# Kernel optimization log

Hardware: AMD Instinct MI355X
Metric: run time of the kernel (lower is better)

The kernel has to match this reference:

```python
import jax, jax.numpy as jnp
import numpy as np

N_FREQS = 6  # PositionEmbedding default used by LISA


def setup_inputs() -> dict:
    key = jax.random.key(0)
    ks = jax.random.split(key, 8)
    B, L, N, D, H = 8, 32768, 2048, 64, 256
    in_dim = 1 * (2 * N_FREQS + 1) + 3 * D  # 13 + 192 = 205

    def w(k, i, o):
        return jax.random.normal(k, (i, o), jnp.float32) * (1.0 / np.sqrt(i))

    return {
        "coord": jax.random.uniform(ks[0], (B, L, 1), jnp.float32),
        "latent": jax.random.normal(ks[1], (B, N, D), jnp.float32),
        "W0": w(ks[2], in_dim, H), "b0": jnp.zeros((H,), jnp.float32),
        "W1": w(ks[3], H, H), "b1": jnp.zeros((H,), jnp.float32),
        "W2": w(ks[4], H, H), "b2": jnp.zeros((H,), jnp.float32),
        "W3": w(ks[5], H, H), "b3": jnp.zeros((H,), jnp.float32),
        "W4": w(ks[6], H, 1), "b4": jnp.zeros((1,), jnp.float32),
    }


def reference(coord, latent, W0, b0, W1, b1, W2, b2, W3, b3, W4, b4):
    B, N, D = latent.shape
    # feat_unfold: concat shifted-prev / self / shifted-next along channels
    feat = jnp.swapaxes(latent, 1, 2)                                   # [B, D, N]
    feat_prev = jnp.concatenate([feat[:, :, :1], feat[:, :, :-1]], axis=2)
    feat_next = jnp.concatenate([feat[:, :, 1:], feat[:, :, -1:]], axis=2)
    feat = jnp.concatenate([feat_prev, feat, feat_next], axis=1)        # [B, 3D, N]

    # grid_sample(bilinear, padding_mode='border', align_corners=False) on a
    # 1-row image: y coordinate 0 hits row 0 exactly, so only x interpolates.
    # torch mapping: ix = ((gx + 1) * W - 1) / 2 with gx = coord*2 - 1
    ix = coord[..., 0] * N - 0.5                                        # [B, L]
    x0 = jnp.floor(ix)
    t = ix - x0                                                         # lerp weight
    i0 = jnp.clip(x0.astype(jnp.int32), 0, N - 1)                       # border clamp
    i1 = jnp.clip(x0.astype(jnp.int32) + 1, 0, N - 1)
    f0 = jnp.take_along_axis(feat, i0[:, None, :], axis=2)              # [B, 3D, L]
    f1 = jnp.take_along_axis(feat, i1[:, None, :], axis=2)
    sampled = (1.0 - t)[:, None, :] * f0 + t[:, None, :] * f1
    sampled = jnp.swapaxes(sampled, 1, 2)                               # [B, L, 3D]

    # positional encoding: [x, sin(f x), cos(f x) for f in 1,2,4,8,16,32]
    freqs = 2.0 ** jnp.arange(N_FREQS, dtype=jnp.float32)
    ang = coord * freqs                                                 # [B, L, 6]
    pe = jnp.stack([jnp.sin(ang), jnp.cos(ang)], axis=-1)
    pe = pe.reshape(ang.shape[0], ang.shape[1], 2 * N_FREQS)            # [B, L, 12]

    inp = jnp.concatenate([coord, pe, sampled], axis=-1)                # [B, L, 205]

    h = jax.nn.relu(inp @ W0 + b0)
    h = jax.nn.relu(h @ W1 + b1)
    h = jax.nn.relu(h @ W2 + b2)
    h = jax.nn.relu(h @ W3 + b3)
    return h @ W4 + b4                                                  # [B, L, 1]
```

## Files before the change

### kernel.cpp

```cpp
#include <hip/hip_runtime.h>
#include <hip/hip_bf16.h>

typedef unsigned short ushort_t;
typedef unsigned int uint_t;
typedef __attribute__((ext_vector_type(8))) short short8;
typedef __attribute__((ext_vector_type(4))) float float4v;
typedef __attribute__((ext_vector_type(4))) uint_t uint4v;

#define NLAT 2048
#define DLAT 64

#define PW_BASE 128
#define PW0_OFF 0
#define PW1_OFF 57344
#define PW2_OFF 122880
#define PW3_OFF 188416

__device__ __forceinline__ float b2f(ushort_t u) {
  union { uint_t i; float f; } v; v.i = ((uint_t)u) << 16; return v.f;
}
__device__ __forceinline__ ushort_t f2b(float f) {
  uint_t x = __float_as_uint(f);
  uint_t r = (x + 0x7fffu + ((x >> 16) & 1u)) >> 16;
  return (ushort_t)r;
}
__device__ __forceinline__ uint_t pack2(float lo, float hi) {
  float2 t; t.x = lo; t.y = hi;
  union { __hip_bfloat162 h; uint_t u; } cv;
  cv.h = __float22bfloat162_rn(t);
  return cv.u;
}
__device__ __forceinline__ int imin(int a, int b) { return a < b ? a : b; }
__device__ __forceinline__ int imax(int a, int b) { return a > b ? a : b; }

__device__ __forceinline__ float ldv(const float* p, long i)    { return p[i]; }
__device__ __forceinline__ float ldv(const ushort_t* p, long i) { return b2f(p[i]); }
__device__ __forceinline__ void stv(float* p, long i, float v)    { p[i] = v; }
__device__ __forceinline__ void stv(ushort_t* p, long i, float v) { p[i] = f2b(v); }

__device__ __forceinline__ float4 load4f(const float* p) { return *(const float4*)p; }
__device__ __forceinline__ float4 load4f(const ushort_t* p) {
  uint2 u = *(const uint2*)p;
  float4 r;
  r.x = b2f((ushort_t)(u.x & 0xffffu)); r.y = b2f((ushort_t)(u.x >> 16));
  r.z = b2f((ushort_t)(u.y & 0xffffu)); r.w = b2f((ushort_t)(u.y >> 16));
  return r;
}

__device__ __forceinline__ void aload(short8& dst, const ushort_t* a) {
  asm volatile("global_load_dwordx4 %0, %1, off" : "=v"(dst) : "v"(a));
}
__device__ __forceinline__ void dsread(short8& dst, const ushort_t* p) {
  asm volatile("ds_read_b128 %0, %1"
               : "=v"(dst)
               : "v"((const __attribute__((address_space(3))) ushort_t*)p));
}
template <int N>
__device__ __forceinline__ void vmwait() {
  if constexpr (N == 0)       asm volatile("s_waitcnt vmcnt(0)"  ::: "memory");
  else if constexpr (N == 4)  asm volatile("s_waitcnt vmcnt(4)"  ::: "memory");
  else if constexpr (N == 8)  asm volatile("s_waitcnt vmcnt(8)"  ::: "memory");
  else                        asm volatile("s_waitcnt vmcnt(12)" ::: "memory");
}
template <int N>
__device__ __forceinline__ void lgwait() {
  if constexpr (N == 0) asm volatile("s_waitcnt lgkmcnt(0)" ::: "memory");
  else                  asm volatile("s_waitcnt lgkmcnt(4)" ::: "memory");
}

__global__ void detect_mode(const ushort_t* __restrict__ lat, int* __restrict__ flag) {
  if (threadIdx.x == 0) *flag = 0;
  __syncthreads();
  int big = 0;
  for (int i = threadIdx.x; i < 1024; i += 64) {
    float v = b2f(lat[i]);
    if (!(fabsf(v) < 1e5f)) big = 1;
  }
  if (__any(big) && threadIdx.x == 0) *flag = 1;
}

template <typename TI>
__device__ __forceinline__ void pack_body(const TI* __restrict__ W0, const TI* __restrict__ W1,
                                          const TI* __restrict__ W2, const TI* __restrict__ W3,
                                          ushort_t* __restrict__ pw)
{
  int g = blockIdx.x * blockDim.x + threadIdx.x;
  if (g >= 31 * 1024) return;
  int lane = g & 63, q = lane >> 4;
  int mt   = (g >> 6) & 15;
  int ktg  = g >> 10;
  const TI* W; ushort_t* dst; int kt, KT; bool isw0 = false;
  if (ktg < 7)       { W = W0; dst = pw + PW0_OFF; kt = ktg;      KT = 7; isw0 = true; }
  else if (ktg < 15) { W = W1; dst = pw + PW1_OFF; kt = ktg - 7;  KT = 8; }
  else if (ktg < 23) { W = W2; dst = pw + PW2_OFF; kt = ktg - 15; KT = 8; }
  else               { W = W3; dst = pw + PW3_OFF; kt = ktg - 23; KT = 8; }
  int col = mt * 16 + (lane & 15);
  uint_t words[4];
#pragma unroll
  for (int h = 0; h < 4; ++h) {
    ushort_t vv[2];
#pragma unroll
    for (int e = 0; e < 2; ++e) {
      int j = 2 * h + e;
      int f = 32 * kt + 16 * (j >> 2) + 4 * q + (j & 3);
      int row = f;
      if (isw0) row = (f < 192) ? (13 + f) : (f == 192 ? 0 : (f <= 204 ? f - 192 : -1));
      vv[e] = (row >= 0) ? f2b(ldv(W, (long)row * 256 + col)) : (ushort_t)0;
    }
    words[h] = (uint_t)vv[0] | ((uint_t)vv[1] << 16);
  }
  uint4 o; o.x = words[0]; o.y = words[1]; o.z = words[2]; o.w = words[3];
  *(uint4*)(dst + ((size_t)(mt * KT + kt) * 64 + lane) * 8) = o;
}

__global__ void pack_w_u(const void* W0, const void* W1, const void* W2, const void* W3,
                         ushort_t* __restrict__ pw, const int* __restrict__ flag)
{
  if (*flag == 1)
    pack_body<float>((const float*)W0, (const float*)W1, (const float*)W2, (const float*)W3, pw);
  else
    pack_body<ushort_t>((const ushort_t*)W0, (const ushort_t*)W1, (const ushort_t*)W2, (const ushort_t*)W3, pw);
}

template <int KT, int BASE, int NEXTKT>
__device__ __forceinline__ void run_layer_fp(const ushort_t* __restrict__ pwl,
                                             const ushort_t* __restrict__ pwl_next,
                                             float4v (&acc)[4][4],
                                             const ushort_t* __restrict__ act,
                                             int lane, int wv, short8 (&Ar)[4][4])
{
#pragma unroll
  for (int m = 0; m < 4; ++m)
#pragma unroll
    for (int i = 0; i < 4; ++i)
      acc[m][i] = (float4v){0.f, 0.f, 0.f, 0.f};

  const ushort_t* abase = pwl + (((size_t)(4 * wv) * KT) * 64 + lane) * 8;
  const ushort_t* nbase = nullptr;
  if constexpr (NEXTKT > 0)
    nbase = pwl_next + (((size_t)(4 * wv) * NEXTKT) * 64 + lane) * 8;

  int boff[4];
#pragma unroll
  for (int i = 0; i < 4; ++i) boff[i] = (((wv + i) & 3) << 12) + (lane << 3);

  short8 B0[4], B1[4];
#pragma unroll
  for (int i = 0; i < 4; ++i) dsread(B0[i], act + boff[i]);

#pragma unroll
  for (int kt = 0; kt < KT; ++kt) {
    short8 (&Bc)[4] = (kt & 1) ? B1 : B0;
    short8 (&Bn)[4] = (kt & 1) ? B0 : B1;
    if (kt + 1 < KT) {
#pragma unroll
      for (int i = 0; i < 4; ++i) dsread(Bn[i], act + boff[i] + (kt + 1) * 512);
    }
    if (kt + 3 < KT) {
#pragma unroll
      for (int m = 0; m < 4; ++m)
        aload(Ar[(BASE + kt + 3) & 3][m], abase + (size_t)(m * KT + kt + 3) * 512);
    } else if constexpr (NEXTKT > 0) {
      const int nk = kt + 3 - KT;
#pragma unroll
      for (int m = 0; m < 4; ++m)
        aload(Ar[(BASE + kt + 3) & 3][m], nbase + (size_t)(m * NEXTKT + nk) * 512);
    }
    if (kt + 1 < KT) lgwait<4>(); else lgwait<0>();
    if (kt + 3 < KT || NEXTKT > 0) vmwait<12>();
    else if (kt == KT - 3)         vmwait<8>();
    else if (kt == KT - 2)         vmwait<4>();
    else                           vmwait<0>();
    __builtin_amdgcn_sched_barrier(0);
    short8 (&Ac)[4] = Ar[(BASE + kt) & 3];
    __builtin_amdgcn_s_setprio(1);
#pragma unroll
    for (int i = 0; i < 4; ++i) {
      acc[0][i] = __builtin_amdgcn_mfma_f32_16x16x32_bf16(Ac[0], Bc[i], acc[0][i], 0, 0, 0);
      acc[1][i] = __builtin_amdgcn_mfma_f32_16x16x32_bf16(Ac[1], Bc[i], acc[1][i], 0, 0, 0);
      acc[2][i] = __builtin_amdgcn_mfma_f32_16x16x32_bf16(Ac[2], Bc[i], acc[2][i], 0, 0, 0);
      acc[3][i] = __builtin_amdgcn_mfma_f32_16x16x32_bf16(Ac[3], Bc[i], acc[3][i], 0, 0, 0);
    }
    __builtin_amdgcn_s_setprio(0);
  }
}

__device__ __forceinline__ void convert_store(float4v (&acc)[4][4],
                                              ushort_t* __restrict__ actN,
                                              const float* __restrict__ bwl,
                                              int lane, int wv, int q)
{
#pragma unroll
  for (int p2 = 0; p2 < 2; ++p2) {
    const float4 bE = *(const float4*)&bwl[wv * 64 + p2 * 32 + 4 * q];
    const float4 bO = *(const float4*)&bwl[wv * 64 + p2 * 32 + 16 + 4 * q];
    const int kt = 2 * wv + p2;
#pragma unroll
    for (int i = 0; i < 4; ++i) {
      const int p = (wv + i) & 3;
      const float4v& aE = acc[2 * p2][i];
      const float4v& aO = acc[2 * p2 + 1][i];
      uint4 o;
      o.x = pack2(fmaxf(aE[0] + bE.x, 0.f), fmaxf(aE[1] + bE.y, 0.f));
      o.y = pack2(fmaxf(aE[2] + bE.z, 0.f), fmaxf(aE[3] + bE.w, 0.f));
      o.z = pack2(fmaxf(aO[0] + bO.x, 0.f), fmaxf(aO[1] + bO.y, 0.f));
      o.w = pack2(fmaxf(aO[2] + bO.z, 0.f), fmaxf(aO[3] + bO.w, 0.f));
      *(uint4*)&actN[(size_t)(p << 12) + kt * 512 + (lane << 3)] = o;
    }
  }
  asm volatile("s_waitcnt lgkmcnt(0)" ::: "memory");
  __builtin_amdgcn_s_barrier();
}

template <typename TI>
__device__ __forceinline__ void fused_body(
    const TI* __restrict__ coord, const TI* __restrict__ latent,
    const TI* __restrict__ bias0, const TI* __restrict__ bias1,
    const TI* __restrict__ bias2, const TI* __restrict__ bias3,
    const TI* __restrict__ W4,    const TI* __restrict__ b4,
    const ushort_t* __restrict__ pw, TI* __restrict__ out,
    ushort_t (*act)[4 * 8 * 64 * 8], float* bw)
{
  const int tid  = threadIdx.x;
  const int lane = tid & 63, q = lane >> 4, m15 = lane & 15;
  const int wv   = tid >> 6;
  const long pbase = (long)blockIdx.x * 64 + wv * 16 + m15;

  for (int i = tid; i < 1281; i += 256) {
    float v;
    if (i < 256)       v = ldv(bias0, i);
    else if (i < 512)  v = ldv(bias1, i - 256);
    else if (i < 768)  v = ldv(bias2, i - 512);
    else if (i < 1024) v = ldv(bias3, i - 768);
    else if (i < 1280) v = ldv(W4, i - 1024);
    else               v = ldv(b4, 0);
    bw[i] = v;
  }

  {
    const long p = pbase;
    float c   = ldv(coord, p);
    float ixv = c * 2048.0f - 0.5f;
    float x0f = floorf(ixv);
    float t   = ixv - x0f;
    int   x0  = (int)x0f;
    int   i0  = imin(imax(x0, 0), NLAT - 1);
    int   i1  = imin(imax(x0 + 1, 0), NLAT - 1);
    float w0 = 1.0f - t, w1 = t;
    int rows0[3] = { imax(i0 - 1, 0), i0, imin(i0 + 1, NLAT - 1) };
    int rows1[3] = { imax(i1 - 1, 0), i1, imin(i1 + 1, NLAT - 1) };
    const TI* lat = latent + (size_t)(p >> 15) * (NLAT * DLAT);
    uint4v hu[7];
#pragma unroll
    for (int tb = 0; tb < 12; ++tb) {
      int region = tb >> 2;
      int d0 = 16 * (tb & 3) + 4 * q;
      float4 a = load4f(lat + (long)rows0[region] * DLAT + d0);
      float4 b = load4f(lat + (long)rows1[region] * DLAT + d0);
      hu[tb >> 1][(tb & 1) * 2 + 0] = pack2(w0 * a.x + w1 * b.x, w0 * a.y + w1 * b.y);
      hu[tb >> 1][(tb & 1) * 2 + 1] = pack2(w0 * a.z + w1 * b.z, w0 * a.w + w1 * b.w);
    }
    float pv[4];
#pragma unroll
    for (int s = 0; s < 4; ++s) {
      int f = 192 + 4 * q + s;
      float v = 0.0f;
      if (f == 192) v = c;
      else if (f <= 204) {
        int i = f - 193;
        float fr = (float)(1 << (i >> 1));
        float ang = c * fr;
        v = (i & 1) ? __cosf(ang) : __sinf(ang);
      }
      pv[s] = v;
    }
    hu[6][0] = pack2(pv[0], pv[1]);
    hu[6][1] = pack2(pv[2], pv[3]);
    hu[6][2] = 0; hu[6][3] = 0;

#pragma unroll
    for (int kt = 0; kt < 7; ++kt)
      *(uint4v*)&act[0][((size_t)(wv * 8 + kt) * 64 + lane) * 8] = hu[kt];
  }
  __syncthreads();

  short8 Ar[4][4];
  {
    const ushort_t* abase = pw + PW0_OFF + (((size_t)(4 * wv) * 7) * 64 + lane) * 8;
#pragma unroll
    for (int s = 0; s < 3; ++s)
#pragma unroll
      for (int m = 0; m < 4; ++m)
        aload(Ar[s][m], abase + (size_t)(m * 7 + s) * 512);
  }

  float4v acc[4][4];

  run_layer_fp<7, 0, 8>(pw + PW0_OFF, pw + PW1_OFF, acc, act[0], lane, wv, Ar);
  convert_store(acc, act[1], bw + 0 * 256, lane, wv, q);
  run_layer_fp<8, 3, 8>(pw + PW1_OFF, pw + PW2_OFF, acc, act[1], lane, wv, Ar);
  convert_store(acc, act[0], bw + 1 * 256, lane, wv, q);
  run_layer_fp<8, 3, 8>(pw + PW2_OFF, pw + PW3_OFF, acc, act[0], lane, wv, Ar);
  convert_store(acc, act[1], bw + 2 * 256, lane, wv, q);
  run_layer_fp<8, 3, 0>(pw + PW3_OFF, nullptr,      acc, act[1], lane, wv, Ar);

  float psum[4] = {0.f, 0.f, 0.f, 0.f};
#pragma unroll
  for (int m = 0; m < 4; ++m) {
    const float4 b3v = *(const float4*)&bw[3 * 256 + wv * 64 + m * 16 + 4 * q];
    const float4 w4v = *(const float4*)&bw[1024 + wv * 64 + m * 16 + 4 * q];
#pragma unroll
    for (int i = 0; i < 4; ++i) {
      float v;
      v = fmaxf(acc[m][i][0] + b3v.x, 0.f); psum[i] += v * w4v.x;
      v = fmaxf(acc[m][i][1] + b3v.y, 0.f); psum[i] += v * w4v.y;
      v = fmaxf(acc[m][i][2] + b3v.z, 0.f); psum[i] += v * w4v.z;
      v = fmaxf(acc[m][i][3] + b3v.w, 0.f); psum[i] += v * w4v.w;
    }
  }
#pragma unroll
  for (int i = 0; i < 4; ++i) {
    psum[i] += __shfl_xor(psum[i], 16, 64);
    psum[i] += __shfl_xor(psum[i], 32, 64);
  }

  asm volatile("" ::: "memory");
  __builtin_amdgcn_s_barrier();
  float* part = (float*)act[0];
  if (lane < 16) {
#pragma unroll
    for (int i = 0; i < 4; ++i) {
      const int p = (wv + i) & 3;
      part[wv * 64 + p * 16 + lane] = psum[i];
    }
  }
  __syncthreads();
  if (tid < 64) {
    float s = part[tid] + part[64 + tid] + part[128 + tid] + part[192 + tid]
            + bw[1280];
    stv(out, (long)blockIdx.x * 64 + tid, s);
  }
}

__global__ __launch_bounds__(256, 2) void lisa_fused_u(
    const void* coord, const void* latent,
    const void* bias0, const void* bias1, const void* bias2, const void* bias3,
    const void* W4,    const void* b4,
    const ushort_t* __restrict__ pw, void* out, const int* __restrict__ flag)
{
  __shared__ __align__(16) ushort_t act[2][4 * 8 * 64 * 8];
  __shared__ __align__(16) float bw[4 * 256 + 256 + 1];

  if (*flag == 1)
    fused_body<float>((const float*)coord, (const float*)latent,
                      (const float*)bias0, (const float*)bias1,
                      (const float*)bias2, (const float*)bias3,
                      (const float*)W4, (const float*)b4,
                      pw, (float*)out, act, bw);
  else
    fused_body<ushort_t>((const ushort_t*)coord, (const ushort_t*)latent,
                         (const ushort_t*)bias0, (const ushort_t*)bias1,
                         (const ushort_t*)bias2, (const ushort_t*)bias3,
                         (const ushort_t*)W4, (const ushort_t*)b4,
                         pw, (ushort_t*)out, act, bw);
}

extern "C" void kernel_launch(void* const* d_in, const int* in_sizes, int n_in,
                              void* d_out, int out_size, void* d_ws, size_t ws_size,
                              hipStream_t stream) {
  int* flag = (int*)d_ws;
  ushort_t* pw = (ushort_t*)d_ws + PW_BASE;

  detect_mode<<<1, 64, 0, stream>>>((const ushort_t*)d_in[1], flag);

  pack_w_u<<<62, 512, 0, stream>>>(d_in[2], d_in[4], d_in[6], d_in[8], pw, flag);

  lisa_fused_u<<<4096, 256, 0, stream>>>(
      d_in[0], d_in[1], d_in[3], d_in[5], d_in[7], d_in[9],
      d_in[10], d_in[11], pw, d_out, flag);
}
```

Baseline: 226.6 us.

## Double points per block to 128 with in-place single activation buffer

```diff
diff --git a/kernel.cpp b/kernel.cpp
--- a/kernel.cpp
+++ b/kernel.cpp
@@ -57,15 +57,11 @@
 }
 template <int N>
 __device__ __forceinline__ void vmwait() {
-  if constexpr (N == 0)       asm volatile("s_waitcnt vmcnt(0)"  ::: "memory");
-  else if constexpr (N == 4)  asm volatile("s_waitcnt vmcnt(4)"  ::: "memory");
-  else if constexpr (N == 8)  asm volatile("s_waitcnt vmcnt(8)"  ::: "memory");
-  else                        asm volatile("s_waitcnt vmcnt(12)" ::: "memory");
-}
-template <int N>
-__device__ __forceinline__ void lgwait() {
-  if constexpr (N == 0) asm volatile("s_waitcnt lgkmcnt(0)" ::: "memory");
-  else                  asm volatile("s_waitcnt lgkmcnt(4)" ::: "memory");
+  if constexpr (N == 0)      asm volatile("s_waitcnt vmcnt(0)" ::: "memory");
+  else                       asm volatile("s_waitcnt vmcnt(4)" ::: "memory");
+}
+__device__ __forceinline__ void lgwait0() {
+  asm volatile("s_waitcnt lgkmcnt(0)" ::: "memory");
 }
 
 __global__ void detect_mode(const ushort_t* __restrict__ lat, int* __restrict__ flag) {
@@ -123,16 +119,16 @@
 }
 
 template <int KT, int BASE, int NEXTKT>
-__device__ __forceinline__ void run_layer_fp(const ushort_t* __restrict__ pwl,
-                                             const ushort_t* __restrict__ pwl_next,
-                                             float4v (&acc)[4][4],
-                                             const ushort_t* __restrict__ act,
-                                             int lane, int wv, short8 (&Ar)[4][4])
+__device__ __forceinline__ void run_layer_w(const ushort_t* __restrict__ pwl,
+                                            const ushort_t* __restrict__ pwl_next,
+                                            float4v (&acc)[4][8],
+                                            const ushort_t* __restrict__ act,
+                                            int lane, int wv, short8 (&Ar)[2][4])
 {
 #pragma unroll
   for (int m = 0; m < 4; ++m)
 #pragma unroll
-    for (int i = 0; i < 4; ++i)
+    for (int i = 0; i < 8; ++i)
       acc[m][i] = (float4v){0.f, 0.f, 0.f, 0.f};
 
   const ushort_t* abase = pwl + (((size_t)(4 * wv) * KT) * 64 + lane) * 8;
@@ -140,55 +136,46 @@
   if constexpr (NEXTKT > 0)
     nbase = pwl_next + (((size_t)(4 * wv) * NEXTKT) * 64 + lane) * 8;
 
-  int boff[4];
-#pragma unroll
-  for (int i = 0; i < 4; ++i) boff[i] = (((wv + i) & 3) << 12) + (lane << 3);
-
-  short8 B0[4], B1[4];
-#pragma unroll
-  for (int i = 0; i < 4; ++i) dsread(B0[i], act + boff[i]);
+  int boff[8];
+#pragma unroll
+  for (int i = 0; i < 8; ++i) boff[i] = (((2 * wv + i) & 7) << 12) + (lane << 3);
+
+  short8 B[8];
 
 #pragma unroll
   for (int kt = 0; kt < KT; ++kt) {
-    short8 (&Bc)[4] = (kt & 1) ? B1 : B0;
-    short8 (&Bn)[4] = (kt & 1) ? B0 : B1;
     if (kt + 1 < KT) {
 #pragma unroll
-      for (int i = 0; i < 4; ++i) dsread(Bn[i], act + boff[i] + (kt + 1) * 512);
-    }
-    if (kt + 3 < KT) {
-#pragma unroll
       for (int m = 0; m < 4; ++m)
-        aload(Ar[(BASE + kt + 3) & 3][m], abase + (size_t)(m * KT + kt + 3) * 512);
+        aload(Ar[(BASE + kt + 1) & 1][m], abase + (size_t)(m * KT + kt + 1) * 512);
     } else if constexpr (NEXTKT > 0) {
-      const int nk = kt + 3 - KT;
 #pragma unroll
       for (int m = 0; m < 4; ++m)
-        aload(Ar[(BASE + kt + 3) & 3][m], nbase + (size_t)(m * NEXTKT + nk) * 512);
-    }
-    if (kt + 1 < KT) lgwait<4>(); else lgwait<0>();
-    if (kt + 3 < KT || NEXTKT > 0) vmwait<12>();
-    else if (kt == KT - 3)         vmwait<8>();
-    else if (kt == KT - 2)         vmwait<4>();
+        aload(Ar[(BASE + kt + 1) & 1][m], nbase + (size_t)(m * NEXTKT) * 512);
+    }
+#pragma unroll
+    for (int i = 0; i < 8; ++i) dsread(B[i], act + boff[i] + kt * 512);
+    lgwait0();
+    if (kt + 1 < KT || NEXTKT > 0) vmwait<4>();
     else                           vmwait<0>();
     __builtin_amdgcn_sched_barrier(0);
-    short8 (&Ac)[4] = Ar[(BASE + kt) & 3];
+    short8 (&Ac)[4] = Ar[(BASE + kt) & 1];
     __builtin_amdgcn_s_setprio(1);
 #pragma unroll
-    for (int i = 0; i < 4; ++i) {
-      acc[0][i] = __builtin_amdgcn_mfma_f32_16x16x32_bf16(Ac[0], Bc[i], acc[0][i], 0, 0, 0);
-      acc[1][i] = __builtin_amdgcn_mfma_f32_16x16x32_bf16(Ac[1], Bc[i], acc[1][i], 0, 0, 0);
-      acc[2][i] = __builtin_amdgcn_mfma_f32_16x16x32_bf16(Ac[2], Bc[i], acc[2][i], 0, 0, 0);
-      acc[3][i] = __builtin_amdgcn_mfma_f32_16x16x32_bf16(Ac[3], Bc[i], acc[3][i], 0, 0, 0);
+    for (int i = 0; i < 8; ++i) {
+      acc[0][i] = __builtin_amdgcn_mfma_f32_16x16x32_bf16(Ac[0], B[i], acc[0][i], 0, 0, 0);
+      acc[1][i] = __builtin_amdgcn_mfma_f32_16x16x32_bf16(Ac[1], B[i], acc[1][i], 0, 0, 0);
+      acc[2][i] = __builtin_amdgcn_mfma_f32_16x16x32_bf16(Ac[2], B[i], acc[2][i], 0, 0, 0);
+      acc[3][i] = __builtin_amdgcn_mfma_f32_16x16x32_bf16(Ac[3], B[i], acc[3][i], 0, 0, 0);
     }
     __builtin_amdgcn_s_setprio(0);
   }
 }
 
-__device__ __forceinline__ void convert_store(float4v (&acc)[4][4],
-                                              ushort_t* __restrict__ actN,
-                                              const float* __restrict__ bwl,
-                                              int lane, int wv, int q)
+__device__ __forceinline__ void convert_store_ip(float4v (&acc)[4][8],
+                                                 ushort_t* __restrict__ act,
+                                                 const float* __restrict__ bwl,
+                                                 int lane, int wv, int q)
 {
 #pragma unroll
   for (int p2 = 0; p2 < 2; ++p2) {
@@ -196,8 +183,8 @@
     const float4 bO = *(const float4*)&bwl[wv * 64 + p2 * 32 + 16 + 4 * q];
     const int kt = 2 * wv + p2;
 #pragma unroll
-    for (int i = 0; i < 4; ++i) {
-      const int p = (wv + i) & 3;
+    for (int i = 0; i < 8; ++i) {
+      const int t = (2 * wv + i) & 7;
       const float4v& aE = acc[2 * p2][i];
       const float4v& aO = acc[2 * p2 + 1][i];
       uint4 o;
@@ -205,10 +192,10 @@
       o.y = pack2(fmaxf(aE[2] + bE.z, 0.f), fmaxf(aE[3] + bE.w, 0.f));
       o.z = pack2(fmaxf(aO[0] + bO.x, 0.f), fmaxf(aO[1] + bO.y, 0.f));
       o.w = pack2(fmaxf(aO[2] + bO.z, 0.f), fmaxf(aO[3] + bO.w, 0.f));
-      *(uint4*)&actN[(size_t)(p << 12) + kt * 512 + (lane << 3)] = o;
-    }
-  }
-  asm volatile("s_waitcnt lgkmcnt(0)" ::: "memory");
+      *(uint4*)&act[(size_t)(t << 12) + kt * 512 + (lane << 3)] = o;
+    }
+  }
+  lgwait0();
   __builtin_amdgcn_s_barrier();
 }
 
@@ -219,12 +206,12 @@
     const TI* __restrict__ bias2, const TI* __restrict__ bias3,
     const TI* __restrict__ W4,    const TI* __restrict__ b4,
     const ushort_t* __restrict__ pw, TI* __restrict__ out,
-    ushort_t (*act)[4 * 8 * 64 * 8], float* bw)
+    ushort_t* act, float* bw)
 {
   const int tid  = threadIdx.x;
   const int lane = tid & 63, q = lane >> 4, m15 = lane & 15;
   const int wv   = tid >> 6;
-  const long pbase = (long)blockIdx.x * 64 + wv * 16 + m15;
+  const long pbase = (long)blockIdx.x * 128 + wv * 32 + m15;
 
   for (int i = tid; i < 1281; i += 256) {
     float v;
@@ -237,8 +224,9 @@
     bw[i] = v;
   }
 
-  {
-    const long p = pbase;
+#pragma unroll
+  for (int g = 0; g < 2; ++g) {
+    const long p = pbase + g * 16;
     float c   = ldv(coord, p);
     float ixv = c * 2048.0f - 0.5f;
     float x0f = floorf(ixv);
@@ -278,39 +266,43 @@
     hu[6][1] = pack2(pv[2], pv[3]);
     hu[6][2] = 0; hu[6][3] = 0;
 
+    const int pt = 2 * wv + g;
 #pragma unroll
     for (int kt = 0; kt < 7; ++kt)
-      *(uint4v*)&act[0][((size_t)(wv * 8 + kt) * 64 + lane) * 8] = hu[kt];
+      *(uint4v*)&act[((size_t)pt << 12) + kt * 512 + (lane << 3)] = hu[kt];
   }
   __syncthreads();
 
-  short8 Ar[4][4];
+  short8 Ar[2][4];
   {
     const ushort_t* abase = pw + PW0_OFF + (((size_t)(4 * wv) * 7) * 64 + lane) * 8;
 #pragma unroll
-    for (int s = 0; s < 3; ++s)
-#pragma unroll
-      for (int m = 0; m < 4; ++m)
-        aload(Ar[s][m], abase + (size_t)(m * 7 + s) * 512);
-  }
-
-  float4v acc[4][4];
-
-  run_layer_fp<7, 0, 8>(pw + PW0_OFF, pw + PW1_OFF, acc, act[0], lane, wv, Ar);
-  convert_store(acc, act[1], bw + 0 * 256, lane, wv, q);
-  run_layer_fp<8, 3, 8>(pw + PW1_OFF, pw + PW2_OFF, acc, act[1], lane, wv, Ar);
-  convert_store(acc, act[0], bw + 1 * 256, lane, wv, q);
-  run_layer_fp<8, 3, 8>(pw + PW2_OFF, pw + PW3_OFF, acc, act[0], lane, wv, Ar);
-  convert_store(acc, act[1], bw + 2 * 256, lane, wv, q);
-  run_layer_fp<8, 3, 0>(pw + PW3_OFF, nullptr,      acc, act[1], lane, wv, Ar);
-
-  float psum[4] = {0.f, 0.f, 0.f, 0.f};
+    for (int m = 0; m < 4; ++m)
+      aload(Ar[0][m], abase + (size_t)(m * 7) * 512);
+  }
+
+  float4v acc[4][8];
+
+  run_layer_w<7, 0, 8>(pw + PW0_OFF, pw + PW1_OFF, acc, act, lane, wv, Ar);
+  __builtin_amdgcn_s_barrier();
+  convert_store_ip(acc, act, bw + 0 * 256, lane, wv, q);
+  run_layer_w<8, 1, 8>(pw + PW1_OFF, pw + PW2_OFF, acc, act, lane, wv, Ar);
+  __builtin_amdgcn_s_barrier();
+  convert_store_ip(acc, act, bw + 1 * 256, lane, wv, q);
+  run_layer_w<8, 1, 8>(pw + PW2_OFF, pw + PW3_OFF, acc, act, lane, wv, Ar);
+  __builtin_amdgcn_s_barrier();
+  convert_store_ip(acc, act, bw + 2 * 256, lane, wv, q);
+  run_layer_w<8, 1, 0>(pw + PW3_OFF, nullptr,      acc, act, lane, wv, Ar);
+
+  float psum[8];
+#pragma unroll
+  for (int i = 0; i < 8; ++i) psum[i] = 0.f;
 #pragma unroll
   for (int m = 0; m < 4; ++m) {
     const float4 b3v = *(const float4*)&bw[3 * 256 + wv * 64 + m * 16 + 4 * q];
     const float4 w4v = *(const float4*)&bw[1024 + wv * 64 + m * 16 + 4 * q];
 #pragma unroll
-    for (int i = 0; i < 4; ++i) {
+    for (int i = 0; i < 8; ++i) {
       float v;
       v = fmaxf(acc[m][i][0] + b3v.x, 0.f); psum[i] += v * w4v.x;
       v = fmaxf(acc[m][i][1] + b3v.y, 0.f); psum[i] += v * w4v.y;
@@ -319,26 +311,26 @@
     }
   }
 #pragma unroll
-  for (int i = 0; i < 4; ++i) {
+  for (int i = 0; i < 8; ++i) {
     psum[i] += __shfl_xor(psum[i], 16, 64);
     psum[i] += __shfl_xor(psum[i], 32, 64);
   }
 
   asm volatile("" ::: "memory");
   __builtin_amdgcn_s_barrier();
-  float* part = (float*)act[0];
+  float* part = (float*)act;
   if (lane < 16) {
 #pragma unroll
-    for (int i = 0; i < 4; ++i) {
-      const int p = (wv + i) & 3;
-      part[wv * 64 + p * 16 + lane] = psum[i];
+    for (int i = 0; i < 8; ++i) {
+      const int t = (2 * wv + i) & 7;
+      part[wv * 128 + t * 16 + lane] = psum[i];
     }
   }
   __syncthreads();
-  if (tid < 64) {
-    float s = part[tid] + part[64 + tid] + part[128 + tid] + part[192 + tid]
+  if (tid < 128) {
+    float s = part[tid] + part[128 + tid] + part[256 + tid] + part[384 + tid]
             + bw[1280];
-    stv(out, (long)blockIdx.x * 64 + tid, s);
+    stv(out, (long)blockIdx.x * 128 + tid, s);
   }
 }
 
@@ -348,7 +340,7 @@
     const void* W4,    const void* b4,
     const ushort_t* __restrict__ pw, void* out, const int* __restrict__ flag)
 {
-  __shared__ __align__(16) ushort_t act[2][4 * 8 * 64 * 8];
+  __shared__ __align__(16) ushort_t act[8 * 8 * 64 * 8];
   __shared__ __align__(16) float bw[4 * 256 + 256 + 1];
 
   if (*flag == 1)
@@ -375,7 +367,7 @@
 
   pack_w_u<<<62, 512, 0, stream>>>(d_in[2], d_in[4], d_in[6], d_in[8], pw, flag);
 
-  lisa_fused_u<<<4096, 256, 0, stream>>>(
+  lisa_fused_u<<<2048, 256, 0, stream>>>(
       d_in[0], d_in[1], d_in[3], d_in[5], d_in[7], d_in[9],
       d_in[10], d_in[11], pw, d_out, flag);
 }
```

After: 266.8 us. 17.7% more time.
